# Optimization experiments

Hardware: AMD Instinct MI355X
Metric: run time of the kernel (lower is better)

## Reference

```python
import jax, jax.numpy as jnp
import numpy as np

K = 11            # filter_size
SPAN = K // 2
BLUR = 4
NUM_ITER = 5      # default num_iter of GaussCRF.forward
UNARY_WEIGHT = 1.0


def avg_pool(x, b):
    # count_include_pad=False avg_pool2d; H,W divisible by b so no padding needed
    B, C, H, W = x.shape
    return x.reshape(B, C, H // b, b, W // b, b).mean(axis=(3, 5))


def extract_patches(x):
    # [B,C,H,W] -> [B,C,K*K,H,W]; patch index i*K+j <-> shift (i-SPAN, j-SPAN), zero padded
    # (matches F.unfold(x, K, 1, SPAN) reshaped to [B,C,K,K,H,W])
    B, C, H, W = x.shape
    xp = jnp.pad(x, ((0, 0), (0, 0), (SPAN, SPAN), (SPAN, SPAN)))
    cols = [xp[:, :, i:i + H, j:j + W] for i in range(K) for j in range(K)]
    return jnp.stack(cols, axis=2)


def shift_mask(H, W, dtype):
    # valid[ij, x, y] = 1 where the shifted pixel (x+dx, y+dy) is in-bounds
    d = jnp.arange(K) - SPAN
    ax = jnp.arange(H)[None, :] + d[:, None]   # [K,H]
    ay = jnp.arange(W)[None, :] + d[:, None]   # [K,W]
    mx = (ax >= 0) & (ax < H)
    my = (ay >= 0) & (ay < W)
    m = mx[:, None, :, None] & my[None, :, None, :]   # [K,K,H,W]
    return m.reshape(K * K, H, W).astype(dtype)


def gauss_kernel(feats):
    # feats: [B,Cf,h,w] (already blurred) -> [B,K*K,h,w]
    # g[b, ij, x, y] = exp(-0.5 * sum_c (f[x+dx,y+dy] - f[x,y])^2), zero where out-of-bounds
    B, C, H, W = feats.shape
    cols = extract_patches(feats)                      # [B,C,K*K,h,w]
    diff2 = (cols - feats[:, :, None]) ** 2
    g = jnp.exp(-0.5 * diff2.sum(axis=1))              # [B,K*K,h,w]
    return g * shift_mask(H, W, feats.dtype)[None]


def reference(unary, img, pos_sdims, col_schan, pos_compat, col_compat, weight):
    B, C, H, W = unary.shape
    dt = unary.dtype

    # pairwise features (mesh is a deterministic buffer)
    mesh = jnp.stack(jnp.meshgrid(jnp.arange(H, dtype=dt), jnp.arange(W, dtype=dt), indexing='ij'))  # [2,H,W]
    pos_feats = jnp.broadcast_to(mesh[None] * pos_sdims, (B, 2, H, W))
    col_feats = img * col_schan                        # use_bias=False

    # merged Gaussian kernel at blurred resolution (merge=True, norm='none')
    g = (pos_compat * gauss_kernel(avg_pool(pos_feats, BLUR))
         + col_compat * gauss_kernel(avg_pool(col_feats, BLUR)))   # [B,K*K,h,w]

    lg_unary = jax.nn.log_softmax(unary, axis=1)       # logsoftmax=True
    pred = lg_unary
    for it in range(NUM_ITER):
        p = avg_pool(pred, BLUR)                       # [B,C,h,w]
        cols = extract_patches(p)                      # [B,C,K*K,h,w]
        msg = jnp.einsum('bkxy,bckxy->bcxy', g, cols)  # local-window message passing
        msg = jax.image.resize(msg, (B, C, H, W), method='bilinear')  # align_corners=False
        pred = (UNARY_WEIGHT - weight) * lg_unary + weight * msg
        if it != NUM_ITER - 1:                         # final_softmax=False
            pred = jax.nn.softmax(pred, axis=1)
    return pred


def setup_inputs() -> dict:
    key = jax.random.key(0)
    k1, k2 = jax.random.split(key)
    B, C, H, W = 2, 21, 512, 512
    return {
        'unary': jax.random.normal(k1, (B, C, H, W), jnp.float32),
        'img': jax.random.uniform(k2, (B, 3, H, W), jnp.float32) * 255.0,  # 0..255 image range (schan=1/13)
        'pos_sdims': jnp.array([1.0 / 3.0], jnp.float32),
        'col_schan': jnp.array([1.0 / 13.0], jnp.float32),
        'pos_compat': jnp.array([3.0], jnp.float32),
        'col_compat': jnp.array([10.0], jnp.float32),
        'weight': jnp.array([0.2], jnp.float32),
    }
```

## Files before the change

kernel.cpp:

```cpp
#include <hip/hip_runtime.h>
#include <cmath>


#define BB 2
#define CC 21
#define HH 512
#define WW 512
#define HP 128
#define WP 128
#define KF 11
#define SPAN 5
#define NB 121
#define NITER 5
#define PLF (HH*WW)
#define PLP (HP*WP)
#define PC 24
#define LSTR 28

__global__ void pool_img_k(const float* __restrict__ img,
                           const float* __restrict__ col_schan,
                           float* __restrict__ cf) {
    int idx = blockIdx.x * blockDim.x + threadIdx.x;
    if (idx >= BB*3*PLP) return;
    int Y  = idx & (WP-1);
    int X  = (idx >> 7) & (HP-1);
    int bc = idx >> 14;
    const float* base = img + ((size_t)bc*HH + X*4)*WW + Y*4;
    float s = 0.f;
    #pragma unroll
    for (int i = 0; i < 4; ++i)
        #pragma unroll
        for (int j = 0; j < 4; ++j)
            s += base[i*WW + j];
    cf[idx] = s * (1.f/16.f) * col_schan[0];
}

__global__ void gauss_k(const float* __restrict__ cf,
                        const float* __restrict__ pos_sdims,
                        const float* __restrict__ pos_compat,
                        const float* __restrict__ col_compat,
                        float* __restrict__ g) {
    int idx = blockIdx.x * blockDim.x + threadIdx.x;
    if (idx >= BB*NB*PLP) return;
    int xy = idx & (PLP-1);
    int t  = idx >> 14;
    int ij = t % NB;
    int b  = t / NB;
    int Y = xy & (WP-1);
    int X = xy >> 7;
    int di = ij / KF - SPAN;
    int dj = ij % KF - SPAN;
    int Xn = X + di, Yn = Y + dj;
    float val = 0.f;
    if (Xn >= 0 && Xn < HP && Yn >= 0 && Yn < WP) {
        const float* cb = cf + (size_t)b*3*PLP;
        int o0 = xy, o = Xn*WP + Yn;
        float d0 = cb[o]         - cb[o0];
        float d1 = cb[PLP + o]   - cb[PLP + o0];
        float d2 = cb[2*PLP + o] - cb[2*PLP + o0];
        float cd2 = d0*d0 + d1*d1 + d2*d2;
        float ps  = 4.f * pos_sdims[0];
        float pd2 = ps*ps * (float)(di*di + dj*dj);
        val = pos_compat[0] * expf(-0.5f*pd2) + col_compat[0] * expf(-0.5f*cd2);
    }
    g[idx] = val;
}

__global__ __launch_bounds__(256) void init_p_k(const float* __restrict__ unary,
                                                float* __restrict__ p) {
    int b = blockIdx.z, tx = blockIdx.y, ty = blockIdx.x;
    int t = threadIdx.x;
    int row = t >> 4, c2 = t & 15;
    int x = tx*16 + row, y = ty*32 + 2*c2;
    size_t base = (size_t)b*CC*PLF + (size_t)x*WW + y;
    float va[CC], vb[CC];
    float ma = -1e30f, mb = -1e30f;
    #pragma unroll
    for (int c = 0; c < CC; ++c) {
        float2 u = *(const float2*)(unary + base + (size_t)c*PLF);
        va[c] = u.x; vb[c] = u.y;
        ma = fmaxf(ma, u.x); mb = fmaxf(mb, u.y);
    }
    float sa = 0.f, sb = 0.f;
    #pragma unroll
    for (int c = 0; c < CC; ++c) { sa += expf(va[c]-ma); sb += expf(vb[c]-mb); }
    float lsa = ma + logf(sa), lsb = mb + logf(sb);
    float out[PC];
    #pragma unroll
    for (int c = 0; c < PC; ++c) out[c] = 0.f;
    #pragma unroll
    for (int c = 0; c < CC; ++c) {
        float sm = (va[c]-lsa) + (vb[c]-lsb);
        sm += __shfl_xor(sm, 1);
        sm += __shfl_xor(sm, 16);
        sm += __shfl_xor(sm, 32);
        out[c] = sm * (1.f/16.f);
    }
    int lane = t & 63;
    if ((lane & 49) == 0) {
        int X = tx*4 + (t >> 6), Y = ty*8 + (c2 >> 1);
        float4* dst = (float4*)(p + ((size_t)(b*HP + X)*WP + Y)*PC);
        const float4* src = (const float4*)out;
        dst[0]=src[0]; dst[1]=src[1]; dst[2]=src[2];
        dst[3]=src[3]; dst[4]=src[4]; dst[5]=src[5];
    }
}

__global__ __launch_bounds__(64) void msg_k(const float* __restrict__ g,
                                            const float* __restrict__ p,
                                            float* __restrict__ msg) {
    int b = blockIdx.z, tx = blockIdx.y, ty = blockIdx.x;
    int t = threadIdx.x;
    int x = t >> 3, y = t & 7;
    __shared__ __align__(16) float pt[18*18*LSTR];
    int X0 = tx*8 - SPAN, Y0 = ty*8 - SPAN;
    const float4* pg = (const float4*)(p + (size_t)b*PLP*PC);
    for (int e = t; e < 18*18*6; e += 64) {
        int pos = e / 6, k = e % 6;
        int r = pos / 18, cl = pos % 18;
        int gX = X0 + r, gY = Y0 + cl;
        float4 v = {0.f,0.f,0.f,0.f};
        if (gX >= 0 && gX < HP && gY >= 0 && gY < WP)
            v = pg[(size_t)(gX*WP + gY)*6 + k];
        *(float4*)(pt + pos*LSTR + k*4) = v;
    }
    __syncthreads();
    int Xg = tx*8 + x, Yg = ty*8 + y;
    const float* gq = g + (size_t)b*NB*PLP + (size_t)Xg*WP + Yg;
    float acc[PC];
    #pragma unroll
    for (int c = 0; c < PC; ++c) acc[c] = 0.f;
    for (int di = 0; di < KF; ++di) {
        const float* prow = pt + (x+di)*18*LSTR + y*LSTR;
        #pragma unroll
        for (int dj = 0; dj < KF; ++dj) {
            float gv = gq[(size_t)(di*KF + dj)*PLP];
            const float4* sp = (const float4*)(prow + dj*LSTR);
            float4 q0 = sp[0], q1 = sp[1], q2 = sp[2];
            float4 q3 = sp[3], q4 = sp[4], q5 = sp[5];
            acc[0]  = fmaf(gv, q0.x, acc[0]);  acc[1]  = fmaf(gv, q0.y, acc[1]);
            acc[2]  = fmaf(gv, q0.z, acc[2]);  acc[3]  = fmaf(gv, q0.w, acc[3]);
            acc[4]  = fmaf(gv, q1.x, acc[4]);  acc[5]  = fmaf(gv, q1.y, acc[5]);
            acc[6]  = fmaf(gv, q1.z, acc[6]);  acc[7]  = fmaf(gv, q1.w, acc[7]);
            acc[8]  = fmaf(gv, q2.x, acc[8]);  acc[9]  = fmaf(gv, q2.y, acc[9]);
            acc[10] = fmaf(gv, q2.z, acc[10]); acc[11] = fmaf(gv, q2.w, acc[11]);
            acc[12] = fmaf(gv, q3.x, acc[12]); acc[13] = fmaf(gv, q3.y, acc[13]);
            acc[14] = fmaf(gv, q3.z, acc[14]); acc[15] = fmaf(gv, q3.w, acc[15]);
            acc[16] = fmaf(gv, q4.x, acc[16]); acc[17] = fmaf(gv, q4.y, acc[17]);
            acc[18] = fmaf(gv, q4.z, acc[18]); acc[19] = fmaf(gv, q4.w, acc[19]);
            acc[20] = fmaf(gv, q5.x, acc[20]);
        }
    }
    float* mb = msg + (size_t)b*CC*PLP + (size_t)Xg*WP + Yg;
    #pragma unroll
    for (int c = 0; c < CC; ++c)
        mb[(size_t)c*PLP] = acc[c];
}

__global__ __launch_bounds__(256) void combine_k(const float* __restrict__ msg,
                                                 const float* __restrict__ unary,
                                                 const float* __restrict__ weight,
                                                 float* __restrict__ pnew,
                                                 float* __restrict__ pred,
                                                 int last) {
    int b = blockIdx.z, tx = blockIdx.y, ty = blockIdx.x;
    int t = threadIdx.x;
    __shared__ float ms[CC][6][10];
    const float* mb = msg + (size_t)b*CC*PLP;
    for (int e = t; e < CC*60; e += 256) {
        int c = e / 60, rr = (e / 10) % 6, cl = e % 10;
        int gX = tx*4 - 1 + rr; gX = gX < 0 ? 0 : (gX > HP-1 ? HP-1 : gX);
        int gY = ty*8 - 1 + cl; gY = gY < 0 ? 0 : (gY > WP-1 ? WP-1 : gY);
        ms[c][rr][cl] = mb[(size_t)c*PLP + gX*WP + gY];
    }
    __syncthreads();
    int row = t >> 4, c2 = t & 15;
    int x = tx*16 + row, y = ty*32 + 2*c2;
    size_t base = (size_t)b*CC*PLF + (size_t)x*WW + y;
    int rs = row & 3, q = row >> 2;
    float fx = (rs == 0) ? 0.625f : (rs == 1) ? 0.875f : (rs == 2) ? 0.125f : 0.375f;
    int i0 = q + (rs >> 1);
    int cs0 = (2*c2) & 3;
    int qc  = (2*c2) >> 2;
    float fya = (cs0 == 0) ? 0.625f : 0.125f;
    float fyb = (cs0 == 0) ? 0.875f : 0.375f;
    int j0 = qc + (cs0 >> 1);
    float gx0 = 1.f - fx;
    float wt = weight[0], uw = 1.f - wt;
    float va[CC], vb[CC];
    float ma = -1e30f, mbx = -1e30f;
    #pragma unroll
    for (int c = 0; c < CC; ++c) {
        float2 u = *(const float2*)(unary + base + (size_t)c*PLF);
        va[c] = u.x; vb[c] = u.y;
        ma = fmaxf(ma, u.x); mbx = fmaxf(mbx, u.y);
    }
    float sa = 0.f, sb = 0.f;
    #pragma unroll
    for (int c = 0; c < CC; ++c) { sa += expf(va[c]-ma); sb += expf(vb[c]-mbx); }
    float lsa = ma + logf(sa), lsb = mbx + logf(sb);
    #pragma unroll
    for (int c = 0; c < CC; ++c) {
        float m00 = ms[c][i0][j0],   m01 = ms[c][i0][j0+1];
        float m10 = ms[c][i0+1][j0], m11 = ms[c][i0+1][j0+1];
        float ca = gx0*m00 + fx*m10;
        float cb = gx0*m01 + fx*m11;
        float mua = (1.f-fya)*ca + fya*cb;
        float mub = (1.f-fyb)*ca + fyb*cb;
        va[c] = uw*(va[c]-lsa) + wt*mua;
        vb[c] = uw*(vb[c]-lsb) + wt*mub;
    }
    if (last) {
        #pragma unroll
        for (int c = 0; c < CC; ++c) {
            float2 o; o.x = va[c]; o.y = vb[c];
            *(float2*)(pred + base + (size_t)c*PLF) = o;
        }
    } else {
        float mma = -1e30f, mmb = -1e30f;
        #pragma unroll
        for (int c = 0; c < CC; ++c) { mma = fmaxf(mma, va[c]); mmb = fmaxf(mmb, vb[c]); }
        float ssa = 0.f, ssb = 0.f;
        #pragma unroll
        for (int c = 0; c < CC; ++c) {
            va[c] = expf(va[c]-mma); ssa += va[c];
            vb[c] = expf(vb[c]-mmb); ssb += vb[c];
        }
        float ia = 1.f/ssa, ib = 1.f/ssb;
        float out[PC];
        #pragma unroll
        for (int c = 0; c < PC; ++c) out[c] = 0.f;
        #pragma unroll
        for (int c = 0; c < CC; ++c) {
            float sm = va[c]*ia + vb[c]*ib;
            sm += __shfl_xor(sm, 1);
            sm += __shfl_xor(sm, 16);
            sm += __shfl_xor(sm, 32);
            out[c] = sm * (1.f/16.f);
        }
        int lane = t & 63;
        if ((lane & 49) == 0) {
            int X = tx*4 + (t >> 6), Y = ty*8 + (c2 >> 1);
            float4* dst = (float4*)(pnew + ((size_t)(b*HP + X)*WP + Y)*PC);
            const float4* src = (const float4*)out;
            dst[0]=src[0]; dst[1]=src[1]; dst[2]=src[2];
            dst[3]=src[3]; dst[4]=src[4]; dst[5]=src[5];
        }
    }
}

extern "C" void kernel_launch(void* const* d_in, const int* in_sizes, int n_in,
                              void* d_out, int out_size, void* d_ws, size_t ws_size,
                              hipStream_t stream) {
    const float* unary      = (const float*)d_in[0];
    const float* img        = (const float*)d_in[1];
    const float* pos_sdims  = (const float*)d_in[2];
    const float* col_schan  = (const float*)d_in[3];
    const float* pos_compat = (const float*)d_in[4];
    const float* col_compat = (const float*)d_in[5];
    const float* weight     = (const float*)d_in[6];
    float* pred = (float*)d_out;
    float* ws   = (float*)d_ws;

    size_t o = 0;
    float* cf  = ws + o;  o += (size_t)BB*3*PLP;
    float* g   = ws + o;  o += (size_t)BB*NB*PLP;
    float* msg = ws + o;  o += (size_t)BB*CC*PLP;
    float* pA  = ws + o;  o += (size_t)BB*PLP*PC;
    float* pB  = ws + o;
    float* pbuf[2] = {pA, pB};

    const int TB = 256;
    hipLaunchKernelGGL(pool_img_k, dim3((BB*3*PLP+TB-1)/TB), dim3(TB), 0, stream,
                       img, col_schan, cf);
    hipLaunchKernelGGL(gauss_k, dim3((BB*NB*PLP+TB-1)/TB), dim3(TB), 0, stream,
                       cf, pos_sdims, pos_compat, col_compat, g);
    hipLaunchKernelGGL(init_p_k, dim3(16, 32, BB), dim3(256), 0, stream,
                       unary, pA);
    for (int it = 0; it < NITER; ++it) {
        hipLaunchKernelGGL(msg_k, dim3(16, 16, BB), dim3(64), 0, stream,
                           g, pbuf[it & 1], msg);
        hipLaunchKernelGGL(combine_k, dim3(16, 32, BB), dim3(256), 0, stream,
                           msg, unary, weight, pbuf[(it + 1) & 1],
                           pred, (it == NITER-1) ? 1 : 0);
    }
}
```

Before: 316.8 us.

## Split msg_k window rows across four waves and tile g per 8x8 block

```diff
diff --git a/kernel.cpp b/kernel.cpp
--- a/kernel.cpp
+++ b/kernel.cpp
@@ -16,6 +16,7 @@
 #define PLP (HP*WP)
 #define PC 24
 #define LSTR 28
+#define RSTR 25
 
 __global__ void pool_img_k(const float* __restrict__ img,
                            const float* __restrict__ col_schan,
@@ -40,21 +41,20 @@
                         const float* __restrict__ pos_compat,
                         const float* __restrict__ col_compat,
                         float* __restrict__ g) {
-    int idx = blockIdx.x * blockDim.x + threadIdx.x;
-    if (idx >= BB*NB*PLP) return;
-    int xy = idx & (PLP-1);
-    int t  = idx >> 14;
-    int ij = t % NB;
-    int b  = t / NB;
-    int Y = xy & (WP-1);
-    int X = xy >> 7;
+    int tile = blockIdx.y;
+    int e = blockIdx.x * blockDim.x + threadIdx.x;
+    if (e >= NB*64) return;
+    int pos = e & 63;
+    int ij  = e >> 6;
+    int tY = tile & 15, tX = (tile >> 4) & 15, b = tile >> 8;
+    int X = tX*8 + (pos >> 3), Y = tY*8 + (pos & 7);
     int di = ij / KF - SPAN;
     int dj = ij % KF - SPAN;
     int Xn = X + di, Yn = Y + dj;
     float val = 0.f;
     if (Xn >= 0 && Xn < HP && Yn >= 0 && Yn < WP) {
         const float* cb = cf + (size_t)b*3*PLP;
-        int o0 = xy, o = Xn*WP + Yn;
+        int o0 = X*WP + Y, o = Xn*WP + Yn;
         float d0 = cb[o]         - cb[o0];
         float d1 = cb[PLP + o]   - cb[PLP + o0];
         float d2 = cb[2*PLP + o] - cb[2*PLP + o0];
@@ -63,7 +63,7 @@
         float pd2 = ps*ps * (float)(di*di + dj*dj);
         val = pos_compat[0] * expf(-0.5f*pd2) + col_compat[0] * expf(-0.5f*cd2);
     }
-    g[idx] = val;
+    g[(size_t)tile*NB*64 + e] = val;
 }
 
 __global__ __launch_bounds__(256) void init_p_k(const float* __restrict__ unary,
@@ -106,16 +106,16 @@
     }
 }
 
-__global__ __launch_bounds__(64) void msg_k(const float* __restrict__ g,
-                                            const float* __restrict__ p,
-                                            float* __restrict__ msg) {
+__global__ __launch_bounds__(256) void msg_k(const float* __restrict__ g,
+                                             const float* __restrict__ p,
+                                             float* __restrict__ msg) {
     int b = blockIdx.z, tx = blockIdx.y, ty = blockIdx.x;
     int t = threadIdx.x;
-    int x = t >> 3, y = t & 7;
     __shared__ __align__(16) float pt[18*18*LSTR];
+    __shared__ float rbuf[3][64][RSTR];
     int X0 = tx*8 - SPAN, Y0 = ty*8 - SPAN;
     const float4* pg = (const float4*)(p + (size_t)b*PLP*PC);
-    for (int e = t; e < 18*18*6; e += 64) {
+    for (int e = t; e < 18*18*6; e += 256) {
         int pos = e / 6, k = e % 6;
         int r = pos / 18, cl = pos % 18;
         int gX = X0 + r, gY = Y0 + cl;
@@ -125,16 +125,19 @@
         *(float4*)(pt + pos*LSTR + k*4) = v;
     }
     __syncthreads();
-    int Xg = tx*8 + x, Yg = ty*8 + y;
-    const float* gq = g + (size_t)b*NB*PLP + (size_t)Xg*WP + Yg;
-    float acc[PC];
-    #pragma unroll
-    for (int c = 0; c < PC; ++c) acc[c] = 0.f;
-    for (int di = 0; di < KF; ++di) {
-        const float* prow = pt + (x+di)*18*LSTR + y*LSTR;
+    int w = t >> 6, lane = t & 63;
+    int x = lane >> 3, y = lane & 7;
+    const float* gt = g + (size_t)((b*16 + tx)*16 + ty)*NB*64 + lane;
+    int d0 = w*3, d1 = (w == 3) ? KF : w*3 + 3;
+    float acc[CC];
+    #pragma unroll
+    for (int c = 0; c < CC; ++c) acc[c] = 0.f;
+    for (int di = d0; di < d1; ++di) {
+        const float* prow = pt + ((x+di)*18 + y)*LSTR;
+        const float* grow = gt + (size_t)(di*KF)*64;
         #pragma unroll
         for (int dj = 0; dj < KF; ++dj) {
-            float gv = gq[(size_t)(di*KF + dj)*PLP];
+            float gv = grow[(size_t)dj*64];
             const float4* sp = (const float4*)(prow + dj*LSTR);
             float4 q0 = sp[0], q1 = sp[1], q2 = sp[2];
             float4 q3 = sp[3], q4 = sp[4], q5 = sp[5];
@@ -151,10 +154,21 @@
             acc[20] = fmaf(gv, q5.x, acc[20]);
         }
     }
-    float* mb = msg + (size_t)b*CC*PLP + (size_t)Xg*WP + Yg;
-    #pragma unroll
-    for (int c = 0; c < CC; ++c)
-        mb[(size_t)c*PLP] = acc[c];
+    if (w > 0) {
+        #pragma unroll
+        for (int c = 0; c < CC; ++c) rbuf[w-1][lane][c] = acc[c];
+    }
+    __syncthreads();
+    if (w == 0) {
+        int Xg = tx*8 + x, Yg = ty*8 + y;
+        float* mb = msg + (size_t)b*CC*PLP + (size_t)Xg*WP + Yg;
+        #pragma unroll
+        for (int c = 0; c < CC; ++c) {
+            float s = ((acc[c] + rbuf[0][lane][c]) + rbuf[1][lane][c])
+                      + rbuf[2][lane][c];
+            mb[(size_t)c*PLP] = s;
+        }
+    }
 }
 
 __global__ __launch_bounds__(256) void combine_k(const float* __restrict__ msg,
@@ -273,12 +287,12 @@
     const int TB = 256;
     hipLaunchKernelGGL(pool_img_k, dim3((BB*3*PLP+TB-1)/TB), dim3(TB), 0, stream,
                        img, col_schan, cf);
-    hipLaunchKernelGGL(gauss_k, dim3((BB*NB*PLP+TB-1)/TB), dim3(TB), 0, stream,
+    hipLaunchKernelGGL(gauss_k, dim3((NB*64+TB-1)/TB, 512), dim3(TB), 0, stream,
                        cf, pos_sdims, pos_compat, col_compat, g);
     hipLaunchKernelGGL(init_p_k, dim3(16, 32, BB), dim3(256), 0, stream,
                        unary, pA);
     for (int it = 0; it < NITER; ++it) {
-        hipLaunchKernelGGL(msg_k, dim3(16, 16, BB), dim3(64), 0, stream,
+        hipLaunchKernelGGL(msg_k, dim3(16, 16, BB), dim3(256), 0, stream,
                            g, pbuf[it & 1], msg);
         hipLaunchKernelGGL(combine_k, dim3(16, 32, BB), dim3(256), 0, stream,
                            msg, unary, weight, pbuf[(it + 1) & 1],
```

Result: faster. 271.2 us (-14.4%).
